# Optimization experiments

Hardware: AMD Instinct MI355X
Metric: run time of the kernel (lower is better)

## Reference

```python
import jax, jax.numpy as jnp
import numpy as np

B, L, R, E, D = 16, 28, 64, 34, 512


def setup_inputs() -> dict:
    key = jax.random.key(0)
    ks = jax.random.split(key, 10)
    logits = jax.random.uniform(ks[0], (B, L, R), dtype=jnp.float32)
    evt_embeddings = jax.random.normal(ks[1], (B, 1, D), dtype=jnp.float32)
    arg_embeddings = jax.random.normal(ks[2], (B, L, D), dtype=jnp.float32)
    # valid-arg counts in [1, L] (used as mask-count multiplier and divisor)
    arg_padding_num = jax.random.randint(ks[3], (B,), 1, L + 1).astype(jnp.float32)
    evt_type_list = jax.random.randint(ks[4], (B,), 0, E)
    s = 1.0 / np.sqrt(D)
    WRT = jax.random.normal(ks[5], (R, D, D), dtype=jnp.float32) * s
    WTT = jax.random.normal(ks[6], (E, D, D), dtype=jnp.float32) * s
    w1 = jax.random.normal(ks[7], (D, 64), dtype=jnp.float32) * s
    b1 = jnp.zeros((64,), dtype=jnp.float32)
    w2 = jax.random.normal(ks[8], (64, 1), dtype=jnp.float32) * (1.0 / 8.0)
    b2 = jnp.zeros((1,), dtype=jnp.float32)
    return {"logits": logits, "evt_embeddings": evt_embeddings,
            "arg_embeddings": arg_embeddings, "arg_padding_num": arg_padding_num,
            "evt_type_list": evt_type_list, "WRT": WRT, "WTT": WTT,
            "w1": w1, "b1": b1, "w2": w2, "b2": b2}


def reference(logits, evt_embeddings, arg_embeddings, arg_padding_num,
              evt_type_list, WRT, WTT, w1, b1, w2, b2):
    # role transition matrix per (event, arg): one-hot/soft select over WRT
    # [B,L,R] x [R,D,D] -> [B,L,D,D]  (dominant, memory-bound intermediate)
    role_mats = jnp.einsum('blr,rde->blde', logits, WRT)
    # event transition matrix: one-hot select over WTT == gather
    evt_mats = WTT[evt_type_list]                      # [B,D,D]
    # event embedding transform: [B,1,D] bmm [B,D,D] -> [B,D]
    evt_trans = jnp.einsum('bd,bde->be', evt_embeddings[:, 0, :], evt_mats)
    # per-arg transform: [B,L,D] bmm [B,L,D,D] -> [B,L,D]
    role_trans = jnp.einsum('bld,blde->ble', arg_embeddings, role_mats)
    # multiply by count, sum over args, divide by count (as in the original)
    role_trans = role_trans * arg_padding_num[:, None, None]
    new_sum = jnp.sum(role_trans, axis=1)              # [B,D]
    div = new_sum / arg_padding_num[:, None]
    graph_embeddings = (div + evt_trans) / 2.0         # [B,D]
    # scorer MLP: Linear(D,64) -> ReLU -> Linear(64,1) -> Sigmoid
    h = jax.nn.relu(graph_embeddings @ w1 + b1)
    score = jax.nn.sigmoid(h @ w2 + b2)                # [B,1]
    return score
```

## Files before the change

### kernel.cpp

```cpp
#include <hip/hip_runtime.h>
#include <math.h>

#define BB 16
#define LL 28
#define RR 64
#define DD 512
#define KK (RR * DD)
#define NROLE 512
#define NEVT 128

__global__ void __launch_bounds__(256) kernel_a(
    const float* __restrict__ logits,
    const float* __restrict__ arg,
    const float* __restrict__ WRT,
    const float* __restrict__ WTT,
    const float* __restrict__ evt_emb,
    const int*   __restrict__ evt_type,
    float* __restrict__ part,
    float* __restrict__ evt_acc)
{
    __shared__ float smem[8192];
    const int t = threadIdx.x;

    if (blockIdx.x >= NROLE) {
        const int blk = blockIdx.x - NROLE;
        const int b  = blk >> 3;
        const int d0 = (blk & 7) * 64;
        const int ty = evt_type[b];
        const float* Wt = WTT + (size_t)ty * DD * DD;
        const int e4 = t & 127;
        const int s  = t >> 7;
        float4 a = {0.f, 0.f, 0.f, 0.f};
#pragma unroll
        for (int db = 0; db < 64; db += 16) {
            float  em[8];
            float4 w[8];
#pragma unroll
            for (int i = 0; i < 8; ++i) {
                const int d = d0 + db + s + 2 * i;
                em[i] = evt_emb[b * DD + d];
                w[i]  = ((const float4*)(Wt + (size_t)d * DD))[e4];
            }
#pragma unroll
            for (int i = 0; i < 8; ++i) {
                a.x = fmaf(em[i], w[i].x, a.x);
                a.y = fmaf(em[i], w[i].y, a.y);
                a.z = fmaf(em[i], w[i].z, a.z);
                a.w = fmaf(em[i], w[i].w, a.w);
            }
        }
        atomicAdd(&evt_acc[b * DD + e4 * 4 + 0], a.x);
        atomicAdd(&evt_acc[b * DD + e4 * 4 + 1], a.y);
        atomicAdd(&evt_acc[b * DD + e4 * 4 + 2], a.z);
        atomicAdd(&evt_acc[b * DD + e4 * 4 + 3], a.w);
        return;
    }

    const int blk = blockIdx.x;
    const int r  = blk >> 3;
    const int d0 = (blk & 7) * 64;

    const int e4 = t & 127;
    const int ks = t >> 7;
    const float4* Wp = (const float4*)(WRT + ((size_t)(r * DD + d0)) * DD);

    float4 w[8];
#pragma unroll
    for (int i = 0; i < 8; ++i)
        w[i] = Wp[(size_t)(ks + 2 * i) * 128 + e4];

    {
        const int d4 = t & 15;
        const int b  = t >> 4;
        const float4* ap = (const float4*)(arg + d0) + d4;
        float4 g = {0.f, 0.f, 0.f, 0.f};
#pragma unroll
        for (int l = 0; l < LL; ++l) {
            const float lg = logits[(b * LL + l) * RR + r];
            const float4 av = ap[(size_t)(b * LL + l) * 128];
            g.x = fmaf(lg, av.x, g.x);
            g.y = fmaf(lg, av.y, g.y);
            g.z = fmaf(lg, av.z, g.z);
            g.w = fmaf(lg, av.w, g.w);
        }
        smem[(4 * d4 + 0) * 16 + b] = g.x;
        smem[(4 * d4 + 1) * 16 + b] = g.y;
        smem[(4 * d4 + 2) * 16 + b] = g.z;
        smem[(4 * d4 + 3) * 16 + b] = g.w;
    }
    __syncthreads();

    const float4* Gl = (const float4*)smem;
    float4 acc[16];
#pragma unroll
    for (int b = 0; b < 16; ++b) acc[b] = make_float4(0.f, 0.f, 0.f, 0.f);

#pragma unroll
    for (int kb = 0; kb < 64; kb += 16) {
        float4 wn[8];
        if (kb + 16 < 64) {
#pragma unroll
            for (int i = 0; i < 8; ++i)
                wn[i] = Wp[(size_t)(kb + 16 + ks + 2 * i) * 128 + e4];
        }
#pragma unroll
        for (int i = 0; i < 8; ++i) {
            const int kk = kb + ks + 2 * i;
            float4 g[4];
            g[0] = Gl[kk * 4 + 0];
            g[1] = Gl[kk * 4 + 1];
            g[2] = Gl[kk * 4 + 2];
            g[3] = Gl[kk * 4 + 3];
            const float* gs = (const float*)g;
#pragma unroll
            for (int b = 0; b < 16; ++b) {
                acc[b].x = fmaf(gs[b], w[i].x, acc[b].x);
                acc[b].y = fmaf(gs[b], w[i].y, acc[b].y);
                acc[b].z = fmaf(gs[b], w[i].z, acc[b].z);
                acc[b].w = fmaf(gs[b], w[i].w, acc[b].w);
            }
        }
#pragma unroll
        for (int i = 0; i < 8; ++i) w[i] = wn[i];
    }
    __syncthreads();

    if (ks == 1) {
        float4* red = (float4*)smem;
#pragma unroll
        for (int b = 0; b < 16; ++b) red[(t - 128) * 16 + b] = acc[b];
    }
    __syncthreads();
    if (ks == 0) {
        const float4* red = (const float4*)smem;
        float4* po = (float4*)part + (size_t)blk * 2048;
#pragma unroll
        for (int b = 0; b < 16; ++b) {
            float4 o = acc[b];
            const float4 q = red[t * 16 + b];
            o.x += q.x; o.y += q.y; o.z += q.z; o.w += q.w;
            po[b * 128 + e4] = o;
        }
    }
}

__global__ void __launch_bounds__(256) kernel_reduce(
    const float* __restrict__ part,
    float* __restrict__ div_acc)
{
    const int ps = blockIdx.x & 31;
    const int oc = blockIdx.x >> 5;
    const int t  = threadIdx.x;
    const int o4 = oc * 256 + t;
    const float4* p4 = (const float4*)part;
    float4 s = {0.f, 0.f, 0.f, 0.f};
#pragma unroll
    for (int i = 0; i < 16; ++i) {
        const int p = ps * 16 + i;
        const float4 v = p4[(size_t)p * 2048 + o4];
        s.x += v.x; s.y += v.y; s.z += v.z; s.w += v.w;
    }
    atomicAdd(&div_acc[o4 * 4 + 0], s.x);
    atomicAdd(&div_acc[o4 * 4 + 1], s.y);
    atomicAdd(&div_acc[o4 * 4 + 2], s.z);
    atomicAdd(&div_acc[o4 * 4 + 3], s.w);
}

__global__ void __launch_bounds__(256) kernel_mlp(
    const float* __restrict__ div_acc,
    const float* __restrict__ evt_acc,
    const float* __restrict__ w1,
    const float* __restrict__ b1,
    const float* __restrict__ w2,
    const float* __restrict__ b2,
    float* __restrict__ out)
{
    __shared__ float hred[256];
    const int b  = blockIdx.x;
    const int t  = threadIdx.x;
    const int j  = t & 63;
    const int dq = t >> 6;
    float hp = 0.f;
#pragma unroll 8
    for (int i = 0; i < 128; ++i) {
        const int d = dq * 128 + i;
        const float g = (div_acc[b * DD + d] + evt_acc[b * DD + d]) * 0.5f;
        hp = fmaf(g, w1[d * 64 + j], hp);
    }
    hred[t] = hp;
    __syncthreads();
    if (t < 64) {
        float h = b1[j] + hred[j] + hred[64 + j] + hred[128 + j] + hred[192 + j];
        h = fmaxf(h, 0.f);
        float v = h * w2[j];
#pragma unroll
        for (int off = 32; off > 0; off >>= 1) v += __shfl_down(v, off, 64);
        if (j == 0) out[b] = 1.f / (1.f + expf(-(v + b2[0])));
    }
}

extern "C" void kernel_launch(void* const* d_in, const int* in_sizes, int n_in,
                              void* d_out, int out_size, void* d_ws, size_t ws_size,
                              hipStream_t stream) {
    const float* logits   = (const float*)d_in[0];
    const float* evt_emb  = (const float*)d_in[1];
    const float* arg_emb  = (const float*)d_in[2];
    const int*   evt_type = (const int*)d_in[4];
    const float* WRT      = (const float*)d_in[5];
    const float* WTT      = (const float*)d_in[6];
    const float* w1       = (const float*)d_in[7];
    const float* b1       = (const float*)d_in[8];
    const float* w2       = (const float*)d_in[9];
    const float* b2       = (const float*)d_in[10];
    float* out = (float*)d_out;

    float* part    = (float*)d_ws;
    float* div_acc = part + (size_t)NROLE * 8192;
    float* evt_acc = div_acc + BB * DD;

    hipMemsetAsync(div_acc, 0, 2 * BB * DD * sizeof(float), stream);

    hipLaunchKernelGGL(kernel_a, dim3(NROLE + NEVT), dim3(256), 0, stream,
                       logits, arg_emb, WRT, WTT, evt_emb, evt_type, part, evt_acc);
    hipLaunchKernelGGL(kernel_reduce, dim3(256), dim3(256), 0, stream,
                       part, div_acc);
    hipLaunchKernelGGL(kernel_mlp, dim3(BB), dim3(256), 0, stream,
                       div_acc, evt_acc, w1, b1, w2, b2, out);
}
```

Baseline: 162.2 us.

## Split role and event blocks finer, replace atomics with deterministic two-stage reduction

```diff
diff --git a/kernel.cpp b/kernel.cpp
--- a/kernel.cpp
+++ b/kernel.cpp
@@ -6,8 +6,9 @@
 #define RR 64
 #define DD 512
 #define KK (RR * DD)
-#define NROLE 512
-#define NEVT 128
+#define NCHUNK 512
+#define NROLE  1024
+#define NEVT   256
 
 __global__ void __launch_bounds__(256) kernel_a(
     const float* __restrict__ logits,
@@ -17,22 +18,23 @@
     const float* __restrict__ evt_emb,
     const int*   __restrict__ evt_type,
     float* __restrict__ part,
-    float* __restrict__ evt_acc)
+    float* __restrict__ evt_part)
 {
     __shared__ float smem[8192];
     const int t = threadIdx.x;
 
     if (blockIdx.x >= NROLE) {
         const int blk = blockIdx.x - NROLE;
-        const int b  = blk >> 3;
-        const int d0 = (blk & 7) * 64;
+        const int b  = blk >> 4;
+        const int dc = blk & 15;
+        const int d0 = dc * 32;
         const int ty = evt_type[b];
         const float* Wt = WTT + (size_t)ty * DD * DD;
         const int e4 = t & 127;
         const int s  = t >> 7;
         float4 a = {0.f, 0.f, 0.f, 0.f};
 #pragma unroll
-        for (int db = 0; db < 64; db += 16) {
+        for (int db = 0; db < 32; db += 16) {
             float  em[8];
             float4 w[8];
 #pragma unroll
@@ -49,25 +51,31 @@
                 a.w = fmaf(em[i], w[i].w, a.w);
             }
         }
-        atomicAdd(&evt_acc[b * DD + e4 * 4 + 0], a.x);
-        atomicAdd(&evt_acc[b * DD + e4 * 4 + 1], a.y);
-        atomicAdd(&evt_acc[b * DD + e4 * 4 + 2], a.z);
-        atomicAdd(&evt_acc[b * DD + e4 * 4 + 3], a.w);
+        float4* sm4 = (float4*)smem;
+        if (s == 1) sm4[e4] = a;
+        __syncthreads();
+        if (s == 0) {
+            const float4 q = sm4[e4];
+            a.x += q.x; a.y += q.y; a.z += q.z; a.w += q.w;
+            ((float4*)evt_part)[(size_t)blk * 128 + e4] = a;
+        }
         return;
     }
 
     const int blk = blockIdx.x;
-    const int r  = blk >> 3;
-    const int d0 = (blk & 7) * 64;
-
-    const int e4 = t & 127;
-    const int ks = t >> 7;
-    const float4* Wp = (const float4*)(WRT + ((size_t)(r * DD + d0)) * DD);
+    const int c  = blk >> 1;
+    const int h  = blk & 1;
+    const int r  = c >> 3;
+    const int d0 = (c & 7) * 64;
+
+    const int e4 = t & 63;
+    const int ks = t >> 6;
+    const float4* Wp = (const float4*)(WRT + ((size_t)(r * DD + d0)) * DD + h * 256);
 
     float4 w[8];
 #pragma unroll
     for (int i = 0; i < 8; ++i)
-        w[i] = Wp[(size_t)(ks + 2 * i) * 128 + e4];
+        w[i] = Wp[(size_t)(ks + 4 * i) * 128 + e4];
 
     {
         const int d4 = t & 15;
@@ -96,16 +104,16 @@
     for (int b = 0; b < 16; ++b) acc[b] = make_float4(0.f, 0.f, 0.f, 0.f);
 
 #pragma unroll
-    for (int kb = 0; kb < 64; kb += 16) {
+    for (int kb = 0; kb < 2; ++kb) {
         float4 wn[8];
-        if (kb + 16 < 64) {
+        if (kb == 0) {
 #pragma unroll
             for (int i = 0; i < 8; ++i)
-                wn[i] = Wp[(size_t)(kb + 16 + ks + 2 * i) * 128 + e4];
+                wn[i] = Wp[(size_t)(ks + 4 * (8 + i)) * 128 + e4];
         }
 #pragma unroll
         for (int i = 0; i < 8; ++i) {
-            const int kk = kb + ks + 2 * i;
+            const int kk = ks + 4 * (kb * 8 + i);
             float4 g[4];
             g[0] = Gl[kk * 4 + 0];
             g[1] = Gl[kk * 4 + 1];
@@ -125,45 +133,81 @@
     }
     __syncthreads();
 
+    float4* sm4 = (float4*)smem;
+    if (ks >= 2) {
+#pragma unroll
+        for (int b = 0; b < 16; ++b) sm4[(ks - 2) * 1024 + e4 * 16 + b] = acc[b];
+    }
+    __syncthreads();
+    if (ks < 2) {
+#pragma unroll
+        for (int b = 0; b < 16; ++b) {
+            const float4 q = sm4[ks * 1024 + e4 * 16 + b];
+            acc[b].x += q.x; acc[b].y += q.y; acc[b].z += q.z; acc[b].w += q.w;
+        }
+    }
+    __syncthreads();
     if (ks == 1) {
-        float4* red = (float4*)smem;
-#pragma unroll
-        for (int b = 0; b < 16; ++b) red[(t - 128) * 16 + b] = acc[b];
+#pragma unroll
+        for (int b = 0; b < 16; ++b) sm4[e4 * 16 + b] = acc[b];
     }
     __syncthreads();
     if (ks == 0) {
-        const float4* red = (const float4*)smem;
-        float4* po = (float4*)part + (size_t)blk * 2048;
+        float4* po = (float4*)part + (size_t)c * 2048;
 #pragma unroll
         for (int b = 0; b < 16; ++b) {
             float4 o = acc[b];
-            const float4 q = red[t * 16 + b];
+            const float4 q = sm4[e4 * 16 + b];
             o.x += q.x; o.y += q.y; o.z += q.z; o.w += q.w;
-            po[b * 128 + e4] = o;
+            po[b * 128 + h * 64 + e4] = o;
         }
     }
 }
 
 __global__ void __launch_bounds__(256) kernel_reduce(
     const float* __restrict__ part,
-    float* __restrict__ div_acc)
+    const float* __restrict__ evt_part,
+    float* __restrict__ div_acc,
+    float* __restrict__ evt_acc)
 {
-    const int ps = blockIdx.x & 31;
-    const int oc = blockIdx.x >> 5;
-    const int t  = threadIdx.x;
-    const int o4 = oc * 256 + t;
-    const float4* p4 = (const float4*)part;
-    float4 s = {0.f, 0.f, 0.f, 0.f};
-#pragma unroll
-    for (int i = 0; i < 16; ++i) {
-        const int p = ps * 16 + i;
-        const float4 v = p4[(size_t)p * 2048 + o4];
-        s.x += v.x; s.y += v.y; s.z += v.z; s.w += v.w;
-    }
-    atomicAdd(&div_acc[o4 * 4 + 0], s.x);
-    atomicAdd(&div_acc[o4 * 4 + 1], s.y);
-    atomicAdd(&div_acc[o4 * 4 + 2], s.z);
-    atomicAdd(&div_acc[o4 * 4 + 3], s.w);
+    const int t = threadIdx.x;
+    if (blockIdx.x < 128) {
+        __shared__ float4 sred[256];
+        const int oo = t & 15;
+        const int pg = t >> 4;
+        const int o4 = blockIdx.x * 16 + oo;
+        const float4* p4 = (const float4*)part;
+        float4 s = {0.f, 0.f, 0.f, 0.f};
+#pragma unroll 8
+        for (int i = 0; i < 32; ++i) {
+            const int p = pg * 32 + i;
+            const float4 v = p4[(size_t)p * 2048 + o4];
+            s.x += v.x; s.y += v.y; s.z += v.z; s.w += v.w;
+        }
+        sred[pg * 16 + oo] = s;
+        __syncthreads();
+        if (t < 16) {
+            float4 tot = sred[t];
+#pragma unroll
+            for (int g = 1; g < 16; ++g) {
+                const float4 v = sred[g * 16 + t];
+                tot.x += v.x; tot.y += v.y; tot.z += v.z; tot.w += v.w;
+            }
+            ((float4*)div_acc)[blockIdx.x * 16 + t] = tot;
+        }
+    } else {
+        const int o4 = (blockIdx.x - 128) * 256 + t;
+        const int b  = o4 >> 7;
+        const int el = o4 & 127;
+        const float4* e4p = (const float4*)evt_part;
+        float4 s = {0.f, 0.f, 0.f, 0.f};
+#pragma unroll
+        for (int dc = 0; dc < 16; ++dc) {
+            const float4 v = e4p[(size_t)(b * 16 + dc) * 128 + el];
+            s.x += v.x; s.y += v.y; s.z += v.z; s.w += v.w;
+        }
+        ((float4*)evt_acc)[o4] = s;
+    }
 }
 
 __global__ void __launch_bounds__(256) kernel_mlp(
@@ -214,16 +258,15 @@
     const float* b2       = (const float*)d_in[10];
     float* out = (float*)d_out;
 
-    float* part    = (float*)d_ws;
-    float* div_acc = part + (size_t)NROLE * 8192;
-    float* evt_acc = div_acc + BB * DD;
-
-    hipMemsetAsync(div_acc, 0, 2 * BB * DD * sizeof(float), stream);
+    float* part     = (float*)d_ws;
+    float* evt_part = part + (size_t)NCHUNK * 8192;
+    float* div_acc  = evt_part + NEVT * DD;
+    float* evt_acc  = div_acc + BB * DD;
 
     hipLaunchKernelGGL(kernel_a, dim3(NROLE + NEVT), dim3(256), 0, stream,
-                       logits, arg_emb, WRT, WTT, evt_emb, evt_type, part, evt_acc);
-    hipLaunchKernelGGL(kernel_reduce, dim3(256), dim3(256), 0, stream,
-                       part, div_acc);
+                       logits, arg_emb, WRT, WTT, evt_emb, evt_type, part, evt_part);
+    hipLaunchKernelGGL(kernel_reduce, dim3(136), dim3(256), 0, stream,
+                       part, evt_part, div_acc, evt_acc);
     hipLaunchKernelGGL(kernel_mlp, dim3(BB), dim3(256), 0, stream,
                        div_acc, evt_acc, w1, b1, w2, b2, out);
 }
```

Result: slower. 165.8 us (+2.2%).
